# Optimization experiments

Hardware: AMD Instinct MI355X
Metric: run time of the kernel (lower is better)

## Reference

```python
import jax, jax.numpy as jnp
import numpy as np

B, L, D_FEAT = 16, 2048, 512
H, D_HID, UNITS = 8, 512, 512


def setup_inputs() -> dict:
    key = jax.random.key(0)
    ks = jax.random.split(key, 8)
    s_feat = 1.0 / np.sqrt(D_FEAT)
    s_hid = 1.0 / np.sqrt(D_HID)
    s_u = 1.0 / np.sqrt(UNITS)
    return {
        "features": jax.random.normal(ks[0], (B, L, D_FEAT), jnp.float32),
        "hidden": jax.random.normal(ks[1], (B, H, D_HID), jnp.float32),
        # Per-head Dense params stacked along a leading head axis.
        "W1": jax.random.normal(ks[2], (H, D_FEAT, UNITS), jnp.float32) * s_feat,
        "b1": jnp.zeros((H, UNITS), jnp.float32),
        "W2": jax.random.normal(ks[3], (H, D_HID, UNITS), jnp.float32) * s_hid,
        "b2": jnp.zeros((H, UNITS), jnp.float32),
        "V": jax.random.normal(ks[4], (H, UNITS), jnp.float32) * s_u,
        "bV": jnp.zeros((H,), jnp.float32),
    }


def reference(features, hidden, W1, b1, W2, b2, V, bV):
    # features: [B, L, Df]; hidden: [B, H, Dh]
    # Per-head: tanh(W1(features) + W2(hidden_h)) -> V -> softmax over L -> weighted sum.
    f_proj = jnp.einsum("bld,hdu->bhlu", features, W1) + b1[None, :, None, :]   # [B,H,L,U]
    h_proj = jnp.einsum("bhd,hdu->bhu", hidden, W2) + b2[None, :, :]            # [B,H,U]
    act = jnp.tanh(f_proj + h_proj[:, :, None, :])                               # [B,H,L,U]
    score = jnp.einsum("bhlu,hu->bhl", act, V) + bV[None, :, None]               # [B,H,L]
    attn = jax.nn.softmax(score, axis=-1)                                        # softmax over L
    context = jnp.einsum("bhl,bld->bhd", attn, features)                         # [B,H,Df]
    # Original stacks weights (each [B,L,1]) along axis=2 -> [B,L,H,1]
    attention_weights = jnp.transpose(attn, (0, 2, 1))[..., None]                # [B,L,H,1]
    return context, attention_weights
```

## Files before the change

### kernel.cpp

```cpp
#include <hip/hip_runtime.h>
#include <hip/hip_bf16.h>

#define B_ 16
#define L_ 2048
#define DF 512
#define H_ 8
#define DH 512
#define U_ 512

typedef unsigned short u16;
typedef __attribute__((ext_vector_type(8))) short bf16x8;
typedef __attribute__((ext_vector_type(4))) float f32x4;

__device__ __forceinline__ u16 f2bf(float x) {
  __hip_bfloat16 h = __float2bfloat16(x);
  u16 u;
  __builtin_memcpy(&u, &h, 2);
  return u;
}

__device__ __forceinline__ void load_lds16(const void* g, void* l) {
  __builtin_amdgcn_global_load_lds(
      (const __attribute__((address_space(1))) void*)g,
      (__attribute__((address_space(3))) void*)l, 16, 0, 0);
}

__device__ __forceinline__ float fast_tanh2(float x) {
  float e = __expf(2.f * x);
  return 1.f - __fdividef(2.f, e + 1.f);
}

__global__ __launch_bounds__(256) void convert_kernel(
    const float* __restrict__ F, u16* __restrict__ Abf,
    const float* __restrict__ W1, u16* __restrict__ W1T) {
  __shared__ float t[32][33];
  if (blockIdx.x < 16384) {
    size_t i = ((size_t)blockIdx.x * 256 + threadIdx.x) * 4;
    float4 v = *(const float4*)(F + i);
    ushort4 o;
    o.x = f2bf(v.x); o.y = f2bf(v.y); o.z = f2bf(v.z); o.w = f2bf(v.w);
    *(ushort4*)(Abf + i) = o;
  } else {
    int bid = blockIdx.x - 16384;
    int d0 = (bid & 15) * 32, u0 = ((bid >> 4) & 15) * 32, h = bid >> 8;
    const float* src = W1 + (size_t)h * DF * U_;
    u16* dst = W1T + (size_t)h * U_ * DF;
#pragma unroll
    for (int i = 0; i < 4; ++i) {
      int idx = threadIdx.x + i * 256;
      int r = idx >> 5, c = idx & 31;
      t[r][c] = src[(size_t)(d0 + r) * U_ + u0 + c];
    }
    __syncthreads();
#pragma unroll
    for (int i = 0; i < 4; ++i) {
      int idx = threadIdx.x + i * 256;
      int r = idx >> 5, c = idx & 31;
      dst[(size_t)(u0 + r) * DF + d0 + c] = f2bf(t[c][r]);
    }
  }
}

__global__ __launch_bounds__(128) void hproj_part_kernel(
    const float* __restrict__ hidden, const float* __restrict__ W2,
    float* __restrict__ partial) {
  int h = blockIdx.x;
  int u = blockIdx.y * 128 + threadIdx.x;
  int d0 = blockIdx.z * 64;
  __shared__ float hs[B_][64];
  for (int idx = threadIdx.x; idx < B_ * 64; idx += 128) {
    int b = idx >> 6, d = idx & 63;
    hs[b][d] = hidden[(size_t)(b * H_ + h) * DH + d0 + d];
  }
  __syncthreads();
  float acc[B_];
#pragma unroll
  for (int b = 0; b < B_; b++) acc[b] = 0.f;
  const float* w2p = W2 + ((size_t)h * DH + d0) * U_ + u;
  for (int d = 0; d < 64; d++) {
    float w = w2p[(size_t)d * U_];
#pragma unroll
    for (int b = 0; b < B_; b++) acc[b] += hs[b][d] * w;
  }
#pragma unroll
  for (int b = 0; b < B_; b++)
    partial[(((size_t)blockIdx.z * B_ + b) * H_ + h) * U_ + u] = acc[b];
}

__global__ __launch_bounds__(256) void hproj_combine_kernel(
    const float* __restrict__ partial, const float* __restrict__ b1,
    const float* __restrict__ b2, float* __restrict__ c) {
  int i = blockIdx.x * 256 + threadIdx.x;
  int hu = i & (H_ * U_ - 1);
  float s = b1[hu] + b2[hu];
#pragma unroll
  for (int z = 0; z < 8; z++) s += partial[(size_t)z * B_ * H_ * U_ + i];
  c[i] = s;
}

#define BKT 64

__global__ __launch_bounds__(512, 2) void score_kernel(
    const u16* __restrict__ Abf, const u16* __restrict__ W1T,
    const float* __restrict__ C, const float* __restrict__ V,
    float* __restrict__ pscore) {
  int gx = blockIdx.x;
  int mt = gx >> 1, ut = gx & 1;
  int l0 = mt * 256, u0 = ut * 256;
  int b = blockIdx.y, h = blockIdx.z;
  int tid = threadIdx.x;
  int lane = tid & 63, wid = tid >> 6;
  int wr = wid >> 2, wc = wid & 3;
  int rl = lane & 15, q = lane >> 4;

  __shared__ u16 As[2][256 * BKT];
  __shared__ u16 Bs[2][256 * BKT];
  __shared__ float redsm[4][256];

  const u16* Fb = Abf + ((size_t)b * L_ + l0) * DF;
  const u16* Wh = W1T + ((size_t)h * U_ + u0) * DF;

  f32x4 acc[8][4];
#pragma unroll
  for (int m = 0; m < 8; ++m)
#pragma unroll
    for (int n = 0; n < 4; ++n)
#pragma unroll
      for (int j = 0; j < 4; ++j) acc[m][n][j] = 0.f;

#define STAGE(bufi, kb)                                                    \
  {                                                                        \
    _Pragma("unroll") for (int i_ = 0; i_ < 4; ++i_) {                     \
      int idx_ = i_ * 512 + tid;                                           \
      int row_ = idx_ >> 3;                                                \
      int ke_ = ((idx_ & 7) ^ (row_ & 7)) << 3;                            \
      load_lds16(Fb + ((size_t)row_ << 9) + (kb) + ke_,                    \
                 &As[bufi][idx_ * 8]);                                     \
      load_lds16(Wh + ((size_t)row_ << 9) + (kb) + ke_,                    \
                 &Bs[bufi][idx_ * 8]);                                     \
    }                                                                      \
  }

  bf16x8 a[4][2], bA[2][2], bB[2][2];

#define RD_A(mb)                                                           \
  {                                                                        \
    _Pragma("unroll") for (int mm = 0; mm < 4; ++mm)                       \
    _Pragma("unroll") for (int ss = 0; ss < 2; ++ss) {                     \
      int rA = wr * 128 + ((mb) + mm) * 16 + rl;                           \
      a[mm][ss] = *(const bf16x8*)&As[c][(rA << 6) +                       \
                                         (((ss * 4 + q) ^ (rA & 7)) << 3)];\
    }                                                                      \
  }

#define RD_B(arr, nb)                                                      \
  {                                                                        \
    _Pragma("unroll") for (int nn = 0; nn < 2; ++nn)                       \
    _Pragma("unroll") for (int ss = 0; ss < 2; ++ss) {                     \
      int rB = wc * 64 + ((nb) + nn) * 16 + rl;                            \
      arr[nn][ss] = *(const bf16x8*)&Bs[c][(rB << 6) +                     \
                                           (((ss * 4 + q) ^ (rB & 7)) << 3)];\
    }                                                                      \
  }

#define MMQ(mb, arr, nb)                                                   \
  {                                                                        \
    _Pragma("unroll") for (int ss = 0; ss < 2; ++ss)                       \
    _Pragma("unroll") for (int mm = 0; mm < 4; ++mm)                       \
    _Pragma("unroll") for (int nn = 0; nn < 2; ++nn)                       \
      acc[(mb) + mm][(nb) + nn] = __builtin_amdgcn_mfma_f32_16x16x32_bf16( \
          a[mm][ss], arr[nn][ss], acc[(mb) + mm][(nb) + nn], 0, 0, 0);     \
  }

  STAGE(0, 0);
  asm volatile("s_waitcnt vmcnt(0)" ::: "memory");
  __builtin_amdgcn_s_barrier();
  __builtin_amdgcn_sched_barrier(0);

  for (int t = 0; t < 8; ++t) {
    int c = t & 1;
    if (t < 7) STAGE(c ^ 1, (t + 1) * BKT);
    RD_A(0);
    RD_B(bA, 0);
    __builtin_amdgcn_s_setprio(1);
    MMQ(0, bA, 0);
    __builtin_amdgcn_s_setprio(0);
    __builtin_amdgcn_s_barrier();
    RD_B(bB, 2);
    __builtin_amdgcn_s_setprio(1);
    MMQ(0, bB, 2);
    __builtin_amdgcn_s_setprio(0);
    __builtin_amdgcn_s_barrier();
    RD_A(4);
    __builtin_amdgcn_s_setprio(1);
    MMQ(4, bB, 2);
    __builtin_amdgcn_s_setprio(0);
    __builtin_amdgcn_s_barrier();
    __builtin_amdgcn_s_setprio(1);
    MMQ(4, bA, 0);
    __builtin_amdgcn_s_setprio(0);
    asm volatile("s_waitcnt vmcnt(0)" ::: "memory");
    __builtin_amdgcn_s_barrier();
    __builtin_amdgcn_sched_barrier(0);
  }
#undef STAGE
#undef RD_A
#undef RD_B
#undef MMQ

  float cu[4], vv[4];
#pragma unroll
  for (int n = 0; n < 4; ++n) {
    int col = u0 + wc * 64 + n * 16 + rl;
    cu[n] = C[(size_t)(b * H_ + h) * U_ + col];
    vv[n] = V[h * U_ + col];
  }
  float part[32];
#pragma unroll
  for (int m = 0; m < 8; ++m)
#pragma unroll
    for (int j = 0; j < 4; ++j) {
      float s = 0.f;
#pragma unroll
      for (int n = 0; n < 4; ++n)
        s += fast_tanh2(acc[m][n][j] + cu[n]) * vv[n];
      part[m * 4 + j] = s;
    }
#pragma unroll
  for (int p = 0; p < 32; ++p) {
    float v = part[p];
    v += __shfl_xor(v, 1, 64);
    v += __shfl_xor(v, 2, 64);
    v += __shfl_xor(v, 4, 64);
    v += __shfl_xor(v, 8, 64);
    part[p] = v;
  }
  if (rl == 0) {
#pragma unroll
    for (int m = 0; m < 8; ++m)
#pragma unroll
      for (int j = 0; j < 4; ++j)
        redsm[wc][wr * 128 + m * 16 + q * 4 + j] = part[m * 4 + j];
  }
  __syncthreads();
  if (tid < 256) {
    float s = redsm[0][tid] + redsm[1][tid] + redsm[2][tid] + redsm[3][tid];
    pscore[((size_t)ut * B_ * H_ + b * H_ + h) * L_ + l0 + tid] = s;
  }
}

__global__ __launch_bounds__(256) void softmax_kernel(
    const float* __restrict__ pscore, float* __restrict__ attn,
    float* __restrict__ aw_out) {
  int bh = blockIdx.x;
  int b = bh / H_, h = bh % H_;
  const float* p0 = pscore + (size_t)bh * L_;
  const float* p1 = pscore + ((size_t)B_ * H_ + bh) * L_;
  __shared__ float sv[L_];
  __shared__ float red[256];

  for (int i = threadIdx.x; i < L_ / 4; i += 256) {
    float4 a = ((const float4*)p0)[i];
    float4 c = ((const float4*)p1)[i];
    a.x += c.x; a.y += c.y; a.z += c.z; a.w += c.w;
    ((float4*)sv)[i] = a;
  }
  __syncthreads();

  float m = -1e30f;
  for (int l = threadIdx.x; l < L_; l += 256) m = fmaxf(m, sv[l]);
  red[threadIdx.x] = m;
  __syncthreads();
  for (int st = 128; st > 0; st >>= 1) {
    if (threadIdx.x < st)
      red[threadIdx.x] = fmaxf(red[threadIdx.x], red[threadIdx.x + st]);
    __syncthreads();
  }
  m = red[0];
  __syncthreads();

  float sum = 0.f;
  for (int l = threadIdx.x; l < L_; l += 256) sum += __expf(sv[l] - m);
  red[threadIdx.x] = sum;
  __syncthreads();
  for (int st = 128; st > 0; st >>= 1) {
    if (threadIdx.x < st) red[threadIdx.x] += red[threadIdx.x + st];
    __syncthreads();
  }
  float inv = 1.f / red[0];

  for (int l = threadIdx.x; l < L_; l += 256) {
    float a = __expf(sv[l] - m) * inv;
    attn[(size_t)bh * L_ + l] = a;
    aw_out[((size_t)b * L_ + l) * H_ + h] = a;
  }
}

__global__ __launch_bounds__(256) void context_part_kernel(
    const float* __restrict__ F, const float* __restrict__ attn,
    float* __restrict__ partial) {
  int b = blockIdx.x;
  int d0 = blockIdx.y * 64;
  int lz = blockIdx.z;
  int td = threadIdx.x & 63;
  int tl = threadIdx.x >> 6;

  __shared__ float as[H_][256];
  for (int idx = threadIdx.x; idx < H_ * 256; idx += 256)
    as[idx >> 8][idx & 255] =
        attn[((size_t)b * H_ + (idx >> 8)) * L_ + lz * 256 + (idx & 255)];
  __syncthreads();

  float acc[H_] = {};
  for (int l = tl; l < 256; l += 4) {
    float f = F[((size_t)b * L_ + lz * 256 + l) * DF + d0 + td];
#pragma unroll
    for (int h = 0; h < H_; h++) acc[h] += as[h][l] * f;
  }

  __shared__ float red[4][H_][64];
#pragma unroll
  for (int h = 0; h < H_; h++) red[tl][h][td] = acc[h];
  __syncthreads();
  if (tl == 0) {
#pragma unroll
    for (int h = 0; h < H_; h++) {
      float v = red[0][h][td] + red[1][h][td] + red[2][h][td] + red[3][h][td];
      partial[(size_t)lz * B_ * H_ * DF + ((size_t)b * H_ + h) * DF + d0 + td] =
          v;
    }
  }
}

__global__ __launch_bounds__(256) void context_combine_kernel(
    const float* __restrict__ partial, float* __restrict__ ctx_out) {
  int i = blockIdx.x * 256 + threadIdx.x;
  float s = 0.f;
#pragma unroll
  for (int z = 0; z < 8; z++) s += partial[(size_t)z * B_ * H_ * DF + i];
  ctx_out[i] = s;
}

extern "C" void kernel_launch(void* const* d_in, const int* in_sizes, int n_in,
                              void* d_out, int out_size, void* d_ws,
                              size_t ws_size, hipStream_t stream) {
  const float* features = (const float*)d_in[0];
  const float* hidden   = (const float*)d_in[1];
  const float* W1       = (const float*)d_in[2];
  const float* b1       = (const float*)d_in[3];
  const float* W2       = (const float*)d_in[4];
  const float* b2       = (const float*)d_in[5];
  const float* V        = (const float*)d_in[6];

  float* out = (float*)d_out;
  float* ctx_out = out;
  float* aw_out  = out + B_ * H_ * DF;

  float* c_buf  = (float*)d_ws;
  float* pscore = c_buf + (size_t)B_ * H_ * U_;
  float* attn   = pscore;
  float* hpart  = pscore;
  float* cpart  = pscore + (size_t)2 * B_ * H_ * L_;
  u16* Abf = (u16*)(cpart + (size_t)8 * B_ * H_ * DF);
  u16* W1T = Abf + (size_t)B_ * L_ * DF;

  convert_kernel<<<16384 + 2048, 256, 0, stream>>>(features, Abf, W1, W1T);
  hproj_part_kernel<<<dim3(H_, U_ / 128, 8), 128, 0, stream>>>(hidden, W2,
                                                               hpart);
  hproj_combine_kernel<<<(B_ * H_ * U_) / 256, 256, 0, stream>>>(hpart, b1, b2,
                                                                 c_buf);
  score_kernel<<<dim3(16, B_, H_), 512, 0, stream>>>(Abf, W1T, c_buf, V,
                                                     pscore);
  softmax_kernel<<<B_ * H_, 256, 0, stream>>>(pscore, attn, aw_out);
  context_part_kernel<<<dim3(B_, DF / 64, 8), 256, 0, stream>>>(features, attn,
                                                                cpart);
  context_combine_kernel<<<(B_ * H_ * DF) / 256, 256, 0, stream>>>(cpart,
                                                                   ctx_out);
}
```

Before: 274.5 us.

## Interleave half-tile global-to-LDS loads with MFMA phases in GEMM main loop

Splits each K-step's A and B LDS staging into half-tile loads that are issued between the four MFMA quadrant phases, using partial vmcnt waits instead of a full drain at the end of each iteration. The wave-to-row/column mapping changes to an interleaved layout so each half-tile is consumed by all waves, and the last iteration is peeled into an epilogue. This aims to spread memory traffic across compute and cut stall time at iteration boundaries, at the cost of more barriers and fragile hand-tuned waitcnt counts.

```diff
diff --git a/kernel.cpp b/kernel.cpp
--- a/kernel.cpp
+++ b/kernel.cpp
@@ -128,90 +128,140 @@
 #pragma unroll
       for (int j = 0; j < 4; ++j) acc[m][n][j] = 0.f;
 
-#define STAGE(bufi, kb)                                                    \
+#define STAGE_A(bufi, half, kb)                                            \
   {                                                                        \
-    _Pragma("unroll") for (int i_ = 0; i_ < 4; ++i_) {                     \
+    _Pragma("unroll") for (int i_ = 0; i_ < 2; ++i_) {                     \
       int idx_ = i_ * 512 + tid;                                           \
       int row_ = idx_ >> 3;                                                \
       int ke_ = ((idx_ & 7) ^ (row_ & 7)) << 3;                            \
-      load_lds16(Fb + ((size_t)row_ << 9) + (kb) + ke_,                    \
-                 &As[bufi][idx_ * 8]);                                     \
-      load_lds16(Wh + ((size_t)row_ << 9) + (kb) + ke_,                    \
-                 &Bs[bufi][idx_ * 8]);                                     \
+      load_lds16(Fb + (((size_t)((half)*128 + row_)) << 9) + (kb) + ke_,   \
+                 &As[bufi][(half)*8192 + idx_ * 8]);                       \
     }                                                                      \
   }
-
-  bf16x8 a[4][2], bA[2][2], bB[2][2];
-
-#define RD_A(mb)                                                           \
+#define STAGE_B(bufi, half, kb)                                            \
+  {                                                                        \
+    _Pragma("unroll") for (int i_ = 0; i_ < 2; ++i_) {                     \
+      int idx_ = i_ * 512 + tid;                                           \
+      int row_ = idx_ >> 3;                                                \
+      int ke_ = ((idx_ & 7) ^ (row_ & 7)) << 3;                            \
+      load_lds16(Wh + (((size_t)((half)*128 + row_)) << 9) + (kb) + ke_,   \
+                 &Bs[bufi][(half)*8192 + idx_ * 8]);                       \
+    }                                                                      \
+  }
+
+  bf16x8 aX[4][2], bA[2][2], bB[2][2];
+
+#define RD_A(mb, bufi)                                                     \
   {                                                                        \
     _Pragma("unroll") for (int mm = 0; mm < 4; ++mm)                       \
     _Pragma("unroll") for (int ss = 0; ss < 2; ++ss) {                     \
-      int rA = wr * 128 + ((mb) + mm) * 16 + rl;                           \
-      a[mm][ss] = *(const bf16x8*)&As[c][(rA << 6) +                       \
-                                         (((ss * 4 + q) ^ (rA & 7)) << 3)];\
+      int rA = ((mb) + mm) * 32 + wr * 16 + rl;                            \
+      aX[mm][ss] = *(const bf16x8*)&As[bufi][(rA << 6) +                   \
+                                    (((ss * 4 + q) ^ (rA & 7)) << 3)];     \
     }                                                                      \
   }
-
-#define RD_B(arr, nb)                                                      \
+#define RD_B(arr, nb, bufi)                                                \
   {                                                                        \
     _Pragma("unroll") for (int nn = 0; nn < 2; ++nn)                       \
     _Pragma("unroll") for (int ss = 0; ss < 2; ++ss) {                     \
-      int rB = wc * 64 + ((nb) + nn) * 16 + rl;                            \
-      arr[nn][ss] = *(const bf16x8*)&Bs[c][(rB << 6) +                     \
-                                           (((ss * 4 + q) ^ (rB & 7)) << 3)];\
+      int rB = ((nb) + nn) * 64 + wc * 16 + rl;                            \
+      arr[nn][ss] = *(const bf16x8*)&Bs[bufi][(rB << 6) +                  \
+                                     (((ss * 4 + q) ^ (rB & 7)) << 3)];    \
     }                                                                      \
   }
-
 #define MMQ(mb, arr, nb)                                                   \
   {                                                                        \
     _Pragma("unroll") for (int ss = 0; ss < 2; ++ss)                       \
     _Pragma("unroll") for (int mm = 0; mm < 4; ++mm)                       \
     _Pragma("unroll") for (int nn = 0; nn < 2; ++nn)                       \
       acc[(mb) + mm][(nb) + nn] = __builtin_amdgcn_mfma_f32_16x16x32_bf16( \
-          a[mm][ss], arr[nn][ss], acc[(mb) + mm][(nb) + nn], 0, 0, 0);     \
-  }
-
-  STAGE(0, 0);
-  asm volatile("s_waitcnt vmcnt(0)" ::: "memory");
+          aX[mm][ss], arr[nn][ss], acc[(mb) + mm][(nb) + nn], 0, 0, 0);    \
+  }
+
+#define LGKM0_SCHED                                                        \
+  asm volatile("s_waitcnt lgkmcnt(0)" ::: "memory");                       \
+  __builtin_amdgcn_sched_barrier(0)
+
+  STAGE_A(0, 0, 0);
+  STAGE_B(0, 0, 0);
+  STAGE_B(0, 1, 0);
+  STAGE_A(0, 1, 0);
+  asm volatile("s_waitcnt vmcnt(4)" ::: "memory");
   __builtin_amdgcn_s_barrier();
-  __builtin_amdgcn_sched_barrier(0);
-
-  for (int t = 0; t < 8; ++t) {
-    int c = t & 1;
-    if (t < 7) STAGE(c ^ 1, (t + 1) * BKT);
-    RD_A(0);
-    RD_B(bA, 0);
+
+#pragma unroll 1
+  for (int t = 0; t < 7; ++t) {
+    int cc = t & 1;
+    int kb = (t + 1) * BKT;
+    RD_A(0, cc);
+    RD_B(bA, 0, cc);
+    STAGE_A(cc ^ 1, 0, kb);
+    __builtin_amdgcn_s_barrier();
+    LGKM0_SCHED;
     __builtin_amdgcn_s_setprio(1);
     MMQ(0, bA, 0);
     __builtin_amdgcn_s_setprio(0);
-    __builtin_amdgcn_s_barrier();
-    RD_B(bB, 2);
+    asm volatile("s_waitcnt vmcnt(4)" ::: "memory");
+    __builtin_amdgcn_s_barrier();
+    RD_B(bB, 2, cc);
+    STAGE_B(cc ^ 1, 0, kb);
+    __builtin_amdgcn_s_barrier();
+    LGKM0_SCHED;
     __builtin_amdgcn_s_setprio(1);
     MMQ(0, bB, 2);
     __builtin_amdgcn_s_setprio(0);
-    __builtin_amdgcn_s_barrier();
-    RD_A(4);
+    asm volatile("s_waitcnt vmcnt(4)" ::: "memory");
+    __builtin_amdgcn_s_barrier();
+    RD_A(4, cc);
+    STAGE_B(cc ^ 1, 1, kb);
+    __builtin_amdgcn_s_barrier();
+    LGKM0_SCHED;
     __builtin_amdgcn_s_setprio(1);
     MMQ(4, bB, 2);
     __builtin_amdgcn_s_setprio(0);
     __builtin_amdgcn_s_barrier();
+    STAGE_A(cc ^ 1, 1, kb);
+    __builtin_amdgcn_s_barrier();
     __builtin_amdgcn_s_setprio(1);
     MMQ(4, bA, 0);
     __builtin_amdgcn_s_setprio(0);
-    asm volatile("s_waitcnt vmcnt(0)" ::: "memory");
-    __builtin_amdgcn_s_barrier();
-    __builtin_amdgcn_sched_barrier(0);
-  }
-#undef STAGE
+    asm volatile("s_waitcnt vmcnt(4)" ::: "memory");
+    __builtin_amdgcn_s_barrier();
+  }
+  RD_A(0, 1);
+  RD_B(bA, 0, 1);
+  __builtin_amdgcn_s_barrier();
+  LGKM0_SCHED;
+  __builtin_amdgcn_s_setprio(1);
+  MMQ(0, bA, 0);
+  __builtin_amdgcn_s_setprio(0);
+  asm volatile("s_waitcnt vmcnt(2)" ::: "memory");
+  __builtin_amdgcn_s_barrier();
+  RD_B(bB, 2, 1);
+  __builtin_amdgcn_s_barrier();
+  LGKM0_SCHED;
+  __builtin_amdgcn_s_setprio(1);
+  MMQ(0, bB, 2);
+  __builtin_amdgcn_s_setprio(0);
+  asm volatile("s_waitcnt vmcnt(0)" ::: "memory");
+  __builtin_amdgcn_s_barrier();
+  RD_A(4, 1);
+  LGKM0_SCHED;
+  __builtin_amdgcn_s_setprio(1);
+  MMQ(4, bB, 2);
+  MMQ(4, bA, 0);
+  __builtin_amdgcn_s_setprio(0);
+#undef STAGE_A
+#undef STAGE_B
 #undef RD_A
 #undef RD_B
 #undef MMQ
+#undef LGKM0_SCHED
 
   float cu[4], vv[4];
 #pragma unroll
   for (int n = 0; n < 4; ++n) {
-    int col = u0 + wc * 64 + n * 16 + rl;
+    int col = u0 + n * 64 + wc * 16 + rl;
     cu[n] = C[(size_t)(b * H_ + h) * U_ + col];
     vv[n] = V[h * U_ + col];
   }
@@ -235,12 +285,13 @@
     v += __shfl_xor(v, 8, 64);
     part[p] = v;
   }
+  __syncthreads();
   if (rl == 0) {
 #pragma unroll
     for (int m = 0; m < 8; ++m)
 #pragma unroll
       for (int j = 0; j < 4; ++j)
-        redsm[wc][wr * 128 + m * 16 + q * 4 + j] = part[m * 4 + j];
+        redsm[wc][m * 32 + wr * 16 + q * 4 + j] = part[m * 4 + j];
   }
   __syncthreads();
   if (tid < 256) {
```

After: 267.4 us. 2.6% less time.

## Rework score GEMM into 4-stage K=32 pipeline with XCD-aware block remap

Applied to the files above, without the earlier changes.

Replaces the double-buffered K=64 main loop in the score kernel with a four-buffer, K=32 ring that keeps three tile loads in flight, using vmcnt-counted waits and a simpler per-step compute. The grid is flattened to 1D and remapped so that consecutive blocks on each XCD share the same batch/L tile, aiming for better L2 reuse of feature rows. The accumulators are seeded with the C bias so the epilogue skips that add. The change trades the old hand-interleaved setprio schedule for deeper prefetch, with more barriers per K step and hand-tuned wait counts that must match the number of loads issued.

```diff
diff --git a/kernel.cpp b/kernel.cpp
--- a/kernel.cpp
+++ b/kernel.cpp
@@ -98,115 +98,32 @@
   c[i] = s;
 }
 
-#define BKT 64
+#define BKQ 32
 
 __global__ __launch_bounds__(512, 2) void score_kernel(
     const u16* __restrict__ Abf, const u16* __restrict__ W1T,
     const float* __restrict__ C, const float* __restrict__ V,
     float* __restrict__ pscore) {
-  int gx = blockIdx.x;
-  int mt = gx >> 1, ut = gx & 1;
-  int l0 = mt * 256, u0 = ut * 256;
-  int b = blockIdx.y, h = blockIdx.z;
+  int bid = blockIdx.x;
+  int logical = (bid & 7) * 256 + (bid >> 3);
+  int mt = logical >> 4;
+  int hu = logical & 15;
+  int h = hu & 7, ut = hu >> 3;
+  int b = mt >> 3;
+  int l0 = (mt & 7) * 256;
+  int u0 = ut * 256;
+
   int tid = threadIdx.x;
   int lane = tid & 63, wid = tid >> 6;
   int wr = wid >> 2, wc = wid & 3;
   int rl = lane & 15, q = lane >> 4;
 
-  __shared__ u16 As[2][256 * BKT];
-  __shared__ u16 Bs[2][256 * BKT];
+  __shared__ u16 As[4][256 * BKQ];
+  __shared__ u16 Bs[4][256 * BKQ];
   __shared__ float redsm[4][256];
 
   const u16* Fb = Abf + ((size_t)b * L_ + l0) * DF;
   const u16* Wh = W1T + ((size_t)h * U_ + u0) * DF;
-
-  f32x4 acc[8][4];
-#pragma unroll
-  for (int m = 0; m < 8; ++m)
-#pragma unroll
-    for (int n = 0; n < 4; ++n)
-#pragma unroll
-      for (int j = 0; j < 4; ++j) acc[m][n][j] = 0.f;
-
-#define STAGE(bufi, kb)                                                    \
-  {                                                                        \
-    _Pragma("unroll") for (int i_ = 0; i_ < 4; ++i_) {                     \
-      int idx_ = i_ * 512 + tid;                                           \
-      int row_ = idx_ >> 3;                                                \
-      int ke_ = ((idx_ & 7) ^ (row_ & 7)) << 3;                            \
-      load_lds16(Fb + ((size_t)row_ << 9) + (kb) + ke_,                    \
-                 &As[bufi][idx_ * 8]);                                     \
-      load_lds16(Wh + ((size_t)row_ << 9) + (kb) + ke_,                    \
-                 &Bs[bufi][idx_ * 8]);                                     \
-    }                                                                      \
-  }
-
-  bf16x8 a[4][2], bA[2][2], bB[2][2];
-
-#define RD_A(mb)                                                           \
-  {                                                                        \
-    _Pragma("unroll") for (int mm = 0; mm < 4; ++mm)                       \
-    _Pragma("unroll") for (int ss = 0; ss < 2; ++ss) {                     \
-      int rA = wr * 128 + ((mb) + mm) * 16 + rl;                           \
-      a[mm][ss] = *(const bf16x8*)&As[c][(rA << 6) +                       \
-                                         (((ss * 4 + q) ^ (rA & 7)) << 3)];\
-    }                                                                      \
-  }
-
-#define RD_B(arr, nb)                                                      \
-  {                                                                        \
-    _Pragma("unroll") for (int nn = 0; nn < 2; ++nn)                       \
-    _Pragma("unroll") for (int ss = 0; ss < 2; ++ss) {                     \
-      int rB = wc * 64 + ((nb) + nn) * 16 + rl;                            \
-      arr[nn][ss] = *(const bf16x8*)&Bs[c][(rB << 6) +                     \
-                                           (((ss * 4 + q) ^ (rB & 7)) << 3)];\
-    }                                                                      \
-  }
-
-#define MMQ(mb, arr, nb)                                                   \
-  {                                                                        \
-    _Pragma("unroll") for (int ss = 0; ss < 2; ++ss)                       \
-    _Pragma("unroll") for (int mm = 0; mm < 4; ++mm)                       \
-    _Pragma("unroll") for (int nn = 0; nn < 2; ++nn)                       \
-      acc[(mb) + mm][(nb) + nn] = __builtin_amdgcn_mfma_f32_16x16x32_bf16( \
-          a[mm][ss], arr[nn][ss], acc[(mb) + mm][(nb) + nn], 0, 0, 0);     \
-  }
-
-  STAGE(0, 0);
-  asm volatile("s_waitcnt vmcnt(0)" ::: "memory");
-  __builtin_amdgcn_s_barrier();
-  __builtin_amdgcn_sched_barrier(0);
-
-  for (int t = 0; t < 8; ++t) {
-    int c = t & 1;
-    if (t < 7) STAGE(c ^ 1, (t + 1) * BKT);
-    RD_A(0);
-    RD_B(bA, 0);
-    __builtin_amdgcn_s_setprio(1);
-    MMQ(0, bA, 0);
-    __builtin_amdgcn_s_setprio(0);
-    __builtin_amdgcn_s_barrier();
-    RD_B(bB, 2);
-    __builtin_amdgcn_s_setprio(1);
-    MMQ(0, bB, 2);
-    __builtin_amdgcn_s_setprio(0);
-    __builtin_amdgcn_s_barrier();
-    RD_A(4);
-    __builtin_amdgcn_s_setprio(1);
-    MMQ(4, bB, 2);
-    __builtin_amdgcn_s_setprio(0);
-    __builtin_amdgcn_s_barrier();
-    __builtin_amdgcn_s_setprio(1);
-    MMQ(4, bA, 0);
-    __builtin_amdgcn_s_setprio(0);
-    asm volatile("s_waitcnt vmcnt(0)" ::: "memory");
-    __builtin_amdgcn_s_barrier();
-    __builtin_amdgcn_sched_barrier(0);
-  }
-#undef STAGE
-#undef RD_A
-#undef RD_B
-#undef MMQ
 
   float cu[4], vv[4];
 #pragma unroll
@@ -215,6 +132,79 @@
     cu[n] = C[(size_t)(b * H_ + h) * U_ + col];
     vv[n] = V[h * U_ + col];
   }
+  f32x4 acc[8][4];
+#pragma unroll
+  for (int m = 0; m < 8; ++m)
+#pragma unroll
+    for (int n = 0; n < 4; ++n)
+#pragma unroll
+      for (int j = 0; j < 4; ++j) acc[m][n][j] = cu[n];
+
+#define STAGE(bufi, kb)                                                    \
+  {                                                                        \
+    _Pragma("unroll") for (int i_ = 0; i_ < 2; ++i_) {                     \
+      int idx_ = i_ * 512 + tid;                                           \
+      int row_ = idx_ >> 2;                                                \
+      int ke_ = ((idx_ & 3) ^ ((row_ >> 1) & 3)) << 3;                     \
+      load_lds16(Fb + ((size_t)row_ << 9) + (kb) + ke_,                    \
+                 &As[bufi][idx_ * 8]);                                     \
+    }                                                                      \
+    _Pragma("unroll") for (int i_ = 0; i_ < 2; ++i_) {                     \
+      int idx_ = i_ * 512 + tid;                                           \
+      int row_ = idx_ >> 2;                                                \
+      int ke_ = ((idx_ & 3) ^ ((row_ >> 1) & 3)) << 3;                     \
+      load_lds16(Wh + ((size_t)row_ << 9) + (kb) + ke_,                    \
+                 &Bs[bufi][idx_ * 8]);                                     \
+    }                                                                      \
+  }
+
+#define COMPUTE(bufi)                                                      \
+  {                                                                        \
+    bf16x8 bF[4];                                                          \
+    _Pragma("unroll") for (int n = 0; n < 4; ++n) {                        \
+      int rB = wc * 64 + n * 16 + rl;                                      \
+      bF[n] = *(const bf16x8*)&Bs[bufi][(rB << 5) +                        \
+                                        ((q ^ ((rB >> 1) & 3)) << 3)];     \
+    }                                                                      \
+    _Pragma("unroll") for (int m = 0; m < 8; ++m) {                        \
+      int rA = wr * 128 + m * 16 + rl;                                     \
+      bf16x8 aF = *(const bf16x8*)&As[bufi][(rA << 5) +                    \
+                                           ((q ^ ((rA >> 1) & 3)) << 3)];  \
+      _Pragma("unroll") for (int n = 0; n < 4; ++n)                        \
+        acc[m][n] = __builtin_amdgcn_mfma_f32_16x16x32_bf16(               \
+            aF, bF[n], acc[m][n], 0, 0, 0);                                \
+    }                                                                      \
+  }
+
+  STAGE(0, 0);
+  STAGE(1, BKQ);
+  STAGE(2, 2 * BKQ);
+
+#pragma unroll 1
+  for (int t = 0; t < 13; ++t) {
+    STAGE((t + 3) & 3, (t + 3) * BKQ);
+    asm volatile("s_waitcnt vmcnt(12)" ::: "memory");
+    __builtin_amdgcn_s_barrier();
+    COMPUTE(t & 3);
+    asm volatile("s_waitcnt lgkmcnt(0)" ::: "memory");
+    __builtin_amdgcn_s_barrier();
+  }
+  asm volatile("s_waitcnt vmcnt(8)" ::: "memory");
+  __builtin_amdgcn_s_barrier();
+  COMPUTE(1);
+  asm volatile("s_waitcnt lgkmcnt(0)" ::: "memory");
+  __builtin_amdgcn_s_barrier();
+  asm volatile("s_waitcnt vmcnt(4)" ::: "memory");
+  __builtin_amdgcn_s_barrier();
+  COMPUTE(2);
+  asm volatile("s_waitcnt lgkmcnt(0)" ::: "memory");
+  __builtin_amdgcn_s_barrier();
+  asm volatile("s_waitcnt vmcnt(0)" ::: "memory");
+  __builtin_amdgcn_s_barrier();
+  COMPUTE(3);
+#undef STAGE
+#undef COMPUTE
+
   float part[32];
 #pragma unroll
   for (int m = 0; m < 8; ++m)
@@ -222,8 +212,7 @@
     for (int j = 0; j < 4; ++j) {
       float s = 0.f;
 #pragma unroll
-      for (int n = 0; n < 4; ++n)
-        s += fast_tanh2(acc[m][n][j] + cu[n]) * vv[n];
+      for (int n = 0; n < 4; ++n) s += fast_tanh2(acc[m][n][j]) * vv[n];
       part[m * 4 + j] = s;
     }
 #pragma unroll
@@ -235,6 +224,7 @@
     v += __shfl_xor(v, 8, 64);
     part[p] = v;
   }
+  __syncthreads();
   if (rl == 0) {
 #pragma unroll
     for (int m = 0; m < 8; ++m)
@@ -369,8 +359,7 @@
                                                                hpart);
   hproj_combine_kernel<<<(B_ * H_ * U_) / 256, 256, 0, stream>>>(hpart, b1, b2,
                                                                  c_buf);
-  score_kernel<<<dim3(16, B_, H_), 512, 0, stream>>>(Abf, W1T, c_buf, V,
-                                                     pscore);
+  score_kernel<<<2048, 512, 0, stream>>>(Abf, W1T, c_buf, V, pscore);
   softmax_kernel<<<B_ * H_, 256, 0, stream>>>(pscore, attn, aw_out);
   context_part_kernel<<<dim3(B_, DF / 64, 8), 256, 0, stream>>>(features, attn,
                                                                 cpart);
```

Result: faster. 268.7 us (-2.1%).
